# Performance work log

Hardware: AMD Instinct MI355X
Metric: run time of the kernel (lower is better)

Reference implementation:

```python
import jax, jax.numpy as jnp
import numpy as np

N_NODES = 50000
N_EDGES = 800000


def sage_conv(x, src, dst, W_l, b_l, W_r, num_nodes):
    """PyG SAGEConv with mean aggregation: out = lin_l(mean_agg(neighbors)) + lin_r(x)."""
    # gather source-node features per edge, scatter-mean into destination nodes
    msg = x[src]                                                   # [E, F]
    agg = jax.ops.segment_sum(msg, dst, num_segments=num_nodes)    # [N, F]
    cnt = jax.ops.segment_sum(jnp.ones((src.shape[0],), x.dtype), dst,
                              num_segments=num_nodes)              # [N]
    agg = agg / jnp.maximum(cnt, 1.0)[:, None]
    return agg @ W_l + b_l + x @ W_r


def setup_inputs() -> dict:
    key = jax.random.key(0)
    ks = jax.random.split(key, 8)
    d_in, d_hid, d_out = 128, 256, 128
    s = lambda k, shape, fan: jax.random.normal(k, shape, jnp.float32) / np.sqrt(fan)
    return {
        "x": jax.random.normal(ks[0], (N_NODES, d_in), jnp.float32),
        "edge_index": jax.random.randint(ks[1], (2, N_EDGES), 0, N_NODES, jnp.int64),
        "W1_l": s(ks[2], (d_in, d_hid), d_in),
        "b1": jnp.zeros((d_hid,), jnp.float32),
        "W1_r": s(ks[3], (d_in, d_hid), d_in),
        "W2_l": s(ks[4], (d_hid, d_out), d_hid),
        "b2": jnp.zeros((d_out,), jnp.float32),
        "W2_r": s(ks[5], (d_hid, d_out), d_hid),
    }


def reference(x, edge_index, W1_l, b1, W1_r, W2_l, b2, W2_r):
    src, dst = edge_index[0], edge_index[1]
    n = x.shape[0]
    h = sage_conv(x, src, dst, W1_l, b1, W1_r, n)
    h = jax.nn.relu(h)  # dropout p=0.0 -> identity
    out = sage_conv(h, src, dst, W2_l, b2, W2_r, n)
    return out
```

## Files before the change

### kernel.cpp

```cpp
#include <hip/hip_runtime.h>
#include <hip/hip_bf16.h>
#include <stdint.h>

#define NN 50000
#define NE 800000
#define NB 196
#define EPB 2048
#define NBLK ((NE + EPB - 1) / EPB)

typedef __attribute__((ext_vector_type(8))) __bf16 bf16x8;
typedef __attribute__((ext_vector_type(4))) float f32x4;
typedef __attribute__((ext_vector_type(4))) int i32x4;

__device__ __forceinline__ float bflo(uint32_t u) { return __uint_as_float(u << 16); }
__device__ __forceinline__ float bfhi(uint32_t u) { return __uint_as_float(u & 0xffff0000u); }
__device__ __forceinline__ uint16_t f2bf(float f) {
    uint32_t u = __float_as_uint(f);
    u += 0x7fffu + ((u >> 16) & 1u);
    return (uint16_t)(u >> 16);
}
__device__ __forceinline__ float bf2f(uint16_t h) { return __uint_as_float(((uint32_t)h) << 16); }

__device__ __forceinline__ int xcd_swz(int bid, int nwg) {
    int q = nwg >> 3, r = nwg & 7;
    int xcd = bid & 7, idx = bid >> 3;
    int base = (xcd < r) ? xcd * (q + 1) : r * (q + 1) + (xcd - r) * q;
    return base + idx;
}

__global__ __launch_bounds__(256) void detect(const uint32_t* __restrict__ xu,
                                              const int* __restrict__ ei,
                                              int* __restrict__ flags) {
    __shared__ int cnt_f, cnt_i;
    if (threadIdx.x == 0) { cnt_f = 0; cnt_i = 0; }
    __syncthreads();
    uint32_t u = xu[threadIdx.x];
    uint32_t lo = u & 0xffffu;
    uint32_t e = (lo >> 7) & 0xffu;
    int ok = (lo == 0u) || (e >= 96u && e <= 150u);
    atomicAdd(&cnt_f, ok);
    if (threadIdx.x < 64) {
        int w = ei[2 * threadIdx.x + 1];
        atomicAdd(&cnt_i, (w != 0) ? 1 : 0);
    }
    __syncthreads();
    if (threadIdx.x == 0) {
        flags[0] = (cnt_f < 192) ? 1 : 0;
        flags[1] = (cnt_i < 4) ? 1 : 0;
    }
}

__global__ __launch_bounds__(256) void hist_pass(const int* __restrict__ ei, const int* __restrict__ flags,
                                                 int* __restrict__ histM) {
    __shared__ int hist[NB];
    for (int i = threadIdx.x; i < NB; i += 256) hist[i] = 0;
    __syncthreads();
    int base = blockIdx.x * EPB;
    int fl = flags[1];
    for (int i = 0; i < EPB; i += 256) {
        int e = base + i + threadIdx.x;
        if (e < NE) {
            int d = fl ? ei[2 * NE + 2 * e] : ei[NE + e];
            atomicAdd(&hist[d >> 8], 1);
        }
    }
    __syncthreads();
    for (int i = threadIdx.x; i < NB; i += 256) histM[i * NBLK + blockIdx.x] = hist[i];
}

__global__ __launch_bounds__(512) void scan_rows(int* __restrict__ histM, int* __restrict__ bucket_tot) {
    __shared__ int sm[512];
    int b = blockIdx.x, t = threadIdx.x;
    int v = (t < NBLK) ? histM[b * NBLK + t] : 0;
    sm[t] = v;
    __syncthreads();
    for (int o = 1; o < 512; o <<= 1) {
        int x = (t >= o) ? sm[t - o] : 0;
        __syncthreads();
        sm[t] += x;
        __syncthreads();
    }
    if (t < NBLK) histM[b * NBLK + t] = sm[t] - v;
    if (t == 511) bucket_tot[b] = sm[511];
}

__global__ __launch_bounds__(256) void scan_tot(const int* __restrict__ bucket_tot, int* __restrict__ bucket_base) {
    __shared__ int sm[256];
    int t = threadIdx.x;
    int v = (t < NB) ? bucket_tot[t] : 0;
    sm[t] = v;
    __syncthreads();
    for (int o = 1; o < 256; o <<= 1) {
        int x = (t >= o) ? sm[t - o] : 0;
        __syncthreads();
        sm[t] += x;
        __syncthreads();
    }
    if (t < NB) bucket_base[t] = sm[t] - v;
    if (t == 0) bucket_base[NB] = NE;
}

__global__ __launch_bounds__(256) void scatter_pass(const int* __restrict__ ei, const int* __restrict__ flags,
                                                    const int* __restrict__ histM, const int* __restrict__ bucket_base,
                                                    uint32_t* __restrict__ staging) {
    __shared__ int curs[NB];
    int blk = blockIdx.x, t = threadIdx.x;
    for (int i = t; i < NB; i += 256) curs[i] = bucket_base[i] + histM[i * NBLK + blk];
    __syncthreads();
    int base = blk * EPB;
    int fl = flags[1];
    for (int i = 0; i < EPB; i += 256) {
        int e = base + i + t;
        if (e < NE) {
            int s, d;
            if (fl) { s = ei[2 * e]; d = ei[2 * NE + 2 * e]; }
            else    { s = ei[e];     d = ei[NE + e]; }
            int p = atomicAdd(&curs[d >> 8], 1);
            staging[p] = ((uint32_t)(d & 0xff) << 16) | (uint32_t)s;
        }
    }
}

__global__ __launch_bounds__(256) void build_csr(const uint32_t* __restrict__ staging,
                                                 const int* __restrict__ bucket_base,
                                                 int* __restrict__ row_start, int* __restrict__ deg,
                                                 float* __restrict__ inv_deg, int* __restrict__ csr) {
    __shared__ int degs[256];
    __shared__ int sm[256];
    __shared__ int curs[256];
    int b = blockIdx.x, t = threadIdx.x;
    int beg = bucket_base[b], cnt = bucket_base[b + 1] - beg;
    degs[t] = 0;
    __syncthreads();
    for (int i = t; i < cnt; i += 256) atomicAdd(&degs[(staging[beg + i] >> 16) & 0xff], 1);
    __syncthreads();
    int d = degs[t];
    sm[t] = d;
    __syncthreads();
    for (int o = 1; o < 256; o <<= 1) {
        int x = (t >= o) ? sm[t - o] : 0;
        __syncthreads();
        sm[t] += x;
        __syncthreads();
    }
    int excl = sm[t] - d;
    curs[t] = excl;
    int node = b * 256 + t;
    if (node < NN) {
        row_start[node] = beg + excl;
        deg[node] = d;
        inv_deg[node] = 1.0f / (float)(d > 0 ? d : 1);
    }
    __syncthreads();
    for (int i = t; i < cnt; i += 256) {
        uint32_t u = staging[beg + i];
        int dl = (u >> 16) & 0xff;
        int p = atomicAdd(&curs[dl], 1);
        csr[beg + p] = (int)(u & 0xffffu);
    }
}

__global__ __launch_bounds__(256) void norm_x(const void* __restrict__ x, const int* __restrict__ flags,
                                              uint32_t* __restrict__ out) {
    int i = blockIdx.x * 256 + threadIdx.x;
    if (flags[0]) {
        f32x4 v = ((const f32x4*)x)[i];
        uint2 o;
        o.x = (uint32_t)f2bf(v[0]) | ((uint32_t)f2bf(v[1]) << 16);
        o.y = (uint32_t)f2bf(v[2]) | ((uint32_t)f2bf(v[3]) << 16);
        ((uint2*)out)[i] = o;
    } else {
        ((uint2*)out)[i] = ((const uint2*)x)[i];
    }
}

__global__ __launch_bounds__(256) void norm_weights_sw(const void* __restrict__ w1l, const void* __restrict__ b1,
                                                       const void* __restrict__ w1r, const void* __restrict__ w2l,
                                                       const void* __restrict__ b2, const void* __restrict__ w2r,
                                                       const int* __restrict__ flags,
                                                       uint16_t* __restrict__ w1l_sw, uint16_t* __restrict__ w1r_sw,
                                                       uint16_t* __restrict__ w2l_sw, uint16_t* __restrict__ w2r_sw,
                                                       uint16_t* __restrict__ bias_buf) {
    int tid = blockIdx.x * 256 + threadIdx.x;
    int fp32 = flags[0];
    if (tid < 16384) {
        int frag = tid >> 6, lane = tid & 63;
        const void* srcw; uint16_t* dst; int N; int fl;
        if (frag < 64)       { srcw = w1l; dst = w1l_sw; N = 256; fl = frag; }
        else if (frag < 128) { srcw = w1r; dst = w1r_sw; N = 256; fl = frag - 64; }
        else if (frag < 192) { srcw = w2l; dst = w2l_sw; N = 128; fl = frag - 128; }
        else                 { srcw = w2r; dst = w2r_sw; N = 128; fl = frag - 192; }
        int NTm = N >> 4;
        int kt = fl / NTm, nt = fl - kt * NTm;
        int k0 = kt * 32 + (lane >> 4) * 8, n = nt * 16 + (lane & 15);
        uint16_t* d = dst + (size_t)fl * 512 + lane * 8;
#pragma unroll
        for (int j = 0; j < 8; j++) {
            int si = (k0 + j) * N + n;
            d[j] = fp32 ? f2bf(((const float*)srcw)[si]) : ((const uint16_t*)srcw)[si];
        }
    } else if (tid < 16384 + 384) {
        int j = tid - 16384;
        const void* s = (j < 256) ? b1 : b2;
        int jj = (j < 256) ? j : j - 256;
        bias_buf[j] = fp32 ? f2bf(((const float*)s)[jj]) : ((const uint16_t*)s)[jj];
    }
}

__global__ __launch_bounds__(256) void agg_mean_v2(const uint32_t* __restrict__ xu,
                                                   const int* __restrict__ row_start,
                                                   const int* __restrict__ deg,
                                                   const int* __restrict__ csr,
                                                   const float* __restrict__ inv_deg,
                                                   uint32_t* __restrict__ outu) {
    int wave = threadIdx.x >> 6, lane = threadIdx.x & 63;
    int half = lane >> 5, l = lane & 31;
    int node = blockIdx.x * 8 + wave * 2 + half;
    int beg = row_start[node], end = beg + deg[node];
    float lx[8], hx[8], ly[8], hy[8];
#pragma unroll
    for (int k = 0; k < 8; k++) { lx[k] = 0.f; hx[k] = 0.f; ly[k] = 0.f; hy[k] = 0.f; }
    int j = beg;
    for (; j + 8 <= end; j += 8) {
        int idx[8];
#pragma unroll
        for (int k = 0; k < 8; k++) idx[k] = csr[j + k];
#pragma unroll
        for (int k = 0; k < 8; k++) {
            uint2 v = *(const uint2*)(xu + (size_t)idx[k] * 64 + l * 2);
            lx[k] += bflo(v.x); hx[k] += bfhi(v.x);
            ly[k] += bflo(v.y); hy[k] += bfhi(v.y);
        }
    }
    for (; j < end; j++) {
        uint2 v = *(const uint2*)(xu + (size_t)csr[j] * 64 + l * 2);
        lx[0] += bflo(v.x); hx[0] += bfhi(v.x);
        ly[0] += bflo(v.y); hy[0] += bfhi(v.y);
    }
    float sc = inv_deg[node];
    float r0 = (((lx[0] + lx[1]) + (lx[2] + lx[3])) + ((lx[4] + lx[5]) + (lx[6] + lx[7]))) * sc;
    float r1 = (((hx[0] + hx[1]) + (hx[2] + hx[3])) + ((hx[4] + hx[5]) + (hx[6] + hx[7]))) * sc;
    float r2 = (((ly[0] + ly[1]) + (ly[2] + ly[3])) + ((ly[4] + ly[5]) + (ly[6] + ly[7]))) * sc;
    float r3 = (((hy[0] + hy[1]) + (hy[2] + hy[3])) + ((hy[4] + hy[5]) + (hy[6] + hy[7]))) * sc;
    uint2 o;
    o.x = (uint32_t)f2bf(r0) | ((uint32_t)f2bf(r1) << 16);
    o.y = (uint32_t)f2bf(r2) | ((uint32_t)f2bf(r3) << 16);
    *(uint2*)(outu + (size_t)node * 64 + l * 2) = o;
}

__global__ __launch_bounds__(256) void agg_final_v2(const uint32_t* __restrict__ tu,
                                                    const int* __restrict__ row_start,
                                                    const int* __restrict__ deg,
                                                    const int* __restrict__ csr,
                                                    const float* __restrict__ inv_deg,
                                                    const f32x4* __restrict__ u,
                                                    f32x4* __restrict__ out) {
    int wave = threadIdx.x >> 6, lane = threadIdx.x & 63;
    int half = lane >> 5, l = lane & 31;
    int node = blockIdx.x * 8 + wave * 2 + half;
    int beg = row_start[node], end = beg + deg[node];
    float lx[8], hx[8], ly[8], hy[8];
#pragma unroll
    for (int k = 0; k < 8; k++) { lx[k] = 0.f; hx[k] = 0.f; ly[k] = 0.f; hy[k] = 0.f; }
    int j = beg;
    for (; j + 8 <= end; j += 8) {
        int idx[8];
#pragma unroll
        for (int k = 0; k < 8; k++) idx[k] = csr[j + k];
#pragma unroll
        for (int k = 0; k < 8; k++) {
            uint2 v = *(const uint2*)(tu + (size_t)idx[k] * 64 + l * 2);
            lx[k] += bflo(v.x); hx[k] += bfhi(v.x);
            ly[k] += bflo(v.y); hy[k] += bfhi(v.y);
        }
    }
    for (; j < end; j++) {
        uint2 v = *(const uint2*)(tu + (size_t)csr[j] * 64 + l * 2);
        lx[0] += bflo(v.x); hx[0] += bfhi(v.x);
        ly[0] += bflo(v.y); hy[0] += bfhi(v.y);
    }
    float sc = inv_deg[node];
    f32x4 uv = u[(size_t)node * 32 + l];
    f32x4 r;
    r[0] = (((lx[0] + lx[1]) + (lx[2] + lx[3])) + ((lx[4] + lx[5]) + (lx[6] + lx[7]))) * sc + uv[0];
    r[1] = (((hx[0] + hx[1]) + (hx[2] + hx[3])) + ((hx[4] + hx[5]) + (hx[6] + hx[7]))) * sc + uv[1];
    r[2] = (((ly[0] + ly[1]) + (ly[2] + ly[3])) + ((ly[4] + ly[5]) + (ly[6] + ly[7]))) * sc + uv[2];
    r[3] = (((hy[0] + hy[1]) + (hy[2] + hy[3])) + ((hy[4] + hy[5]) + (hy[6] + hy[7]))) * sc + uv[3];
    out[(size_t)node * 32 + l] = r;
}

__global__ __launch_bounds__(256) void gemm1_v2(const uint16_t* __restrict__ A1,
                                                const uint16_t* __restrict__ A2,
                                                const uint16_t* __restrict__ W1sw,
                                                const uint16_t* __restrict__ W2sw,
                                                const uint16_t* __restrict__ bias,
                                                uint16_t* __restrict__ C) {
    __shared__ __align__(16) uint16_t cs[64][72];
    int wg = xcd_swz(blockIdx.x, 3128);
    int rg = wg >> 2, cg = wg & 3;
    int wave = threadIdx.x >> 6, lane = threadIdx.x & 63;
    int wr = wave >> 1, wc = wave & 1;
    int m = lane & 15, q = lane >> 4;
    int rowbase = rg * 64 + wr * 32;
    int gnt0 = cg * 4 + wc * 2;

    int ar[2];
#pragma unroll
    for (int rf = 0; rf < 2; rf++) {
        int r = rowbase + rf * 16 + m;
        ar[rf] = (r < NN) ? r : (NN - 1);
    }

    f32x4 acc[2][2];
#pragma unroll
    for (int rf = 0; rf < 2; rf++)
#pragma unroll
        for (int nt = 0; nt < 2; nt++)
#pragma unroll
            for (int i = 0; i < 4; i++) acc[rf][nt][i] = 0.f;

    {
        bf16x8 B[4][2];
#pragma unroll
        for (int kt = 0; kt < 4; kt++)
#pragma unroll
            for (int nt = 0; nt < 2; nt++)
                B[kt][nt] = *(const bf16x8*)(W1sw + ((size_t)(kt * 16 + gnt0 + nt)) * 512 + lane * 8);
#pragma unroll
        for (int kt = 0; kt < 4; kt++) {
            bf16x8 a0 = *(const bf16x8*)(A1 + (size_t)ar[0] * 128 + kt * 32 + q * 8);
            bf16x8 a1 = *(const bf16x8*)(A1 + (size_t)ar[1] * 128 + kt * 32 + q * 8);
#pragma unroll
            for (int nt = 0; nt < 2; nt++) {
                acc[0][nt] = __builtin_amdgcn_mfma_f32_16x16x32_bf16(a0, B[kt][nt], acc[0][nt], 0, 0, 0);
                acc[1][nt] = __builtin_amdgcn_mfma_f32_16x16x32_bf16(a1, B[kt][nt], acc[1][nt], 0, 0, 0);
            }
        }
    }
    asm volatile("" ::: "memory");
    {
        bf16x8 B[4][2];
#pragma unroll
        for (int kt = 0; kt < 4; kt++)
#pragma unroll
            for (int nt = 0; nt < 2; nt++)
                B[kt][nt] = *(const bf16x8*)(W2sw + ((size_t)(kt * 16 + gnt0 + nt)) * 512 + lane * 8);
#pragma unroll
        for (int kt = 0; kt < 4; kt++) {
            bf16x8 a0 = *(const bf16x8*)(A2 + (size_t)ar[0] * 128 + kt * 32 + q * 8);
            bf16x8 a1 = *(const bf16x8*)(A2 + (size_t)ar[1] * 128 + kt * 32 + q * 8);
#pragma unroll
            for (int nt = 0; nt < 2; nt++) {
                acc[0][nt] = __builtin_amdgcn_mfma_f32_16x16x32_bf16(a0, B[kt][nt], acc[0][nt], 0, 0, 0);
                acc[1][nt] = __builtin_amdgcn_mfma_f32_16x16x32_bf16(a1, B[kt][nt], acc[1][nt], 0, 0, 0);
            }
        }
    }

#pragma unroll
    for (int rf = 0; rf < 2; rf++)
#pragma unroll
        for (int nt = 0; nt < 2; nt++) {
            int coll = wc * 32 + nt * 16 + m;
            float bv = bf2f(bias[cg * 64 + coll]);
#pragma unroll
            for (int i = 0; i < 4; i++) {
                float v = fmaxf(acc[rf][nt][i] + bv, 0.f);
                cs[wr * 32 + rf * 16 + q * 4 + i][coll] = f2bf(v);
            }
        }
    __syncthreads();
    int tt = threadIdx.x;
#pragma unroll
    for (int rr = 0; rr < 2; rr++) {
        int row = rr * 32 + (tt >> 3);
        int grow = rg * 64 + row;
        if (grow < NN)
            *(i32x4*)(C + (size_t)grow * 256 + cg * 64 + (tt & 7) * 8) =
                *(const i32x4*)&cs[row][(tt & 7) * 8];
    }
}

__global__ __launch_bounds__(256) void gemm2_v2(const uint16_t* __restrict__ A,
                                                const uint16_t* __restrict__ W1sw,
                                                const uint16_t* __restrict__ W2sw,
                                                const uint16_t* __restrict__ bias,
                                                uint16_t* __restrict__ T,
                                                float* __restrict__ U) {
    __shared__ __align__(16) uint16_t ts[64][72];
    __shared__ __align__(16) float us[64][68];
    int wg = xcd_swz(blockIdx.x, 1564);
    int rg = wg >> 1, cg = wg & 1;
    int wave = threadIdx.x >> 6, lane = threadIdx.x & 63;
    int wr = wave >> 1, wc = wave & 1;
    int m = lane & 15, q = lane >> 4;
    int rowbase = rg * 64 + wr * 32;
    int gnt0 = cg * 4 + wc * 2;

    int ar[2];
#pragma unroll
    for (int rf = 0; rf < 2; rf++) {
        int r = rowbase + rf * 16 + m;
        ar[rf] = (r < NN) ? r : (NN - 1);
    }

    f32x4 acc1[2][2], acc2[2][2];
#pragma unroll
    for (int rf = 0; rf < 2; rf++)
#pragma unroll
        for (int nt = 0; nt < 2; nt++)
#pragma unroll
            for (int i = 0; i < 4; i++) { acc1[rf][nt][i] = 0.f; acc2[rf][nt][i] = 0.f; }

    {
        bf16x8 B[8][2];
#pragma unroll
        for (int kt = 0; kt < 8; kt++)
#pragma unroll
            for (int nt = 0; nt < 2; nt++)
                B[kt][nt] = *(const bf16x8*)(W1sw + ((size_t)(kt * 8 + gnt0 + nt)) * 512 + lane * 8);
#pragma unroll
        for (int kt = 0; kt < 8; kt++) {
            bf16x8 a0 = *(const bf16x8*)(A + (size_t)ar[0] * 256 + kt * 32 + q * 8);
            bf16x8 a1 = *(const bf16x8*)(A + (size_t)ar[1] * 256 + kt * 32 + q * 8);
#pragma unroll
            for (int nt = 0; nt < 2; nt++) {
                acc1[0][nt] = __builtin_amdgcn_mfma_f32_16x16x32_bf16(a0, B[kt][nt], acc1[0][nt], 0, 0, 0);
                acc1[1][nt] = __builtin_amdgcn_mfma_f32_16x16x32_bf16(a1, B[kt][nt], acc1[1][nt], 0, 0, 0);
            }
        }
    }
    asm volatile("" ::: "memory");
    {
        bf16x8 B[8][2];
#pragma unroll
        for (int kt = 0; kt < 8; kt++)
#pragma unroll
            for (int nt = 0; nt < 2; nt++)
                B[kt][nt] = *(const bf16x8*)(W2sw + ((size_t)(kt * 8 + gnt0 + nt)) * 512 + lane * 8);
#pragma unroll
        for (int kt = 0; kt < 8; kt++) {
            bf16x8 a0 = *(const bf16x8*)(A + (size_t)ar[0] * 256 + kt * 32 + q * 8);
            bf16x8 a1 = *(const bf16x8*)(A + (size_t)ar[1] * 256 + kt * 32 + q * 8);
#pragma unroll
            for (int nt = 0; nt < 2; nt++) {
                acc2[0][nt] = __builtin_amdgcn_mfma_f32_16x16x32_bf16(a0, B[kt][nt], acc2[0][nt], 0, 0, 0);
                acc2[1][nt] = __builtin_amdgcn_mfma_f32_16x16x32_bf16(a1, B[kt][nt], acc2[1][nt], 0, 0, 0);
            }
        }
    }

#pragma unroll
    for (int rf = 0; rf < 2; rf++)
#pragma unroll
        for (int nt = 0; nt < 2; nt++) {
            int coll = wc * 32 + nt * 16 + m;
            float bv = bf2f(bias[cg * 64 + coll]);
#pragma unroll
            for (int i = 0; i < 4; i++) {
                int rl = wr * 32 + rf * 16 + q * 4 + i;
                ts[rl][coll] = f2bf(acc1[rf][nt][i]);
                us[rl][coll] = acc2[rf][nt][i] + bv;
            }
        }
    __syncthreads();
    int tt = threadIdx.x;
#pragma unroll
    for (int rr = 0; rr < 2; rr++) {
        int row = rr * 32 + (tt >> 3);
        int grow = rg * 64 + row;
        if (grow < NN)
            *(i32x4*)(T + (size_t)grow * 128 + cg * 64 + (tt & 7) * 8) =
                *(const i32x4*)&ts[row][(tt & 7) * 8];
    }
#pragma unroll
    for (int rr = 0; rr < 4; rr++) {
        int row = rr * 16 + (tt >> 4);
        int grow = rg * 64 + row;
        if (grow < NN)
            *(f32x4*)(U + (size_t)grow * 128 + cg * 64 + (tt & 15) * 4) =
                *(const f32x4*)&us[row][(tt & 15) * 4];
    }
}

extern "C" void kernel_launch(void* const* d_in, const int* in_sizes, int n_in,
                              void* d_out, int out_size, void* d_ws, size_t ws_size,
                              hipStream_t stream) {
    const void* x_raw  = d_in[0];
    const int*  ei     = (const int*)d_in[1];
    const void* W1l    = d_in[2];
    const void* b1     = d_in[3];
    const void* W1r    = d_in[4];
    const void* W2l    = d_in[5];
    const void* b2     = d_in[6];
    const void* W2r    = d_in[7];

    uint8_t* ws = (uint8_t*)d_ws;
    size_t off = 0;
    auto alloc = [&](size_t b) -> void* {
        void* p = ws + off;
        off += (b + 255) & ~(size_t)255;
        return p;
    };
    int*      flags       = (int*)alloc(256);
    int*      histM       = (int*)alloc((size_t)NB * NBLK * 4);
    int*      bucket_tot  = (int*)alloc((NB + 4) * 4);
    int*      bucket_base = (int*)alloc((NB + 4) * 4);
    int*      deg         = (int*)alloc((size_t)NN * 4);
    float*    inv_deg     = (float*)alloc((size_t)NN * 4);
    int*      row_start   = (int*)alloc((size_t)NN * 4);
    int*      csr         = (int*)alloc((size_t)NE * 4);
    uint32_t* xb          = (uint32_t*)alloc((size_t)NN * 64 * 4);
    uint16_t* bias_buf    = (uint16_t*)alloc(384 * 2);
    uint16_t* agg         = (uint16_t*)alloc((size_t)NN * 128 * 2);
    uint16_t* h           = (uint16_t*)alloc((size_t)NN * 256 * 2);
    uint16_t* t           = (uint16_t*)alloc((size_t)NN * 128 * 2);
    float*    u           = (float*)alloc((size_t)NN * 128 * 4);
    uint16_t* w1l_sw      = (uint16_t*)alloc(128 * 256 * 2);
    uint16_t* w1r_sw      = (uint16_t*)alloc(128 * 256 * 2);
    uint16_t* w2l_sw      = (uint16_t*)alloc(256 * 128 * 2);
    uint16_t* w2r_sw      = (uint16_t*)alloc(256 * 128 * 2);

    uint32_t* staging = (uint32_t*)h;

    detect<<<1, 256, 0, stream>>>((const uint32_t*)x_raw, ei, flags);

    hist_pass<<<NBLK, 256, 0, stream>>>(ei, flags, histM);
    scan_rows<<<NB, 512, 0, stream>>>(histM, bucket_tot);
    scan_tot<<<1, 256, 0, stream>>>(bucket_tot, bucket_base);
    scatter_pass<<<NBLK, 256, 0, stream>>>(ei, flags, histM, bucket_base, staging);
    build_csr<<<NB, 256, 0, stream>>>(staging, bucket_base, row_start, deg, inv_deg, csr);

    norm_x<<<(NN * 32 + 255) / 256, 256, 0, stream>>>(x_raw, flags, xb);
    norm_weights_sw<<<66, 256, 0, stream>>>(W1l, b1, W1r, W2l, b2, W2r, flags,
                                            w1l_sw, w1r_sw, w2l_sw, w2r_sw, bias_buf);

    agg_mean_v2<<<NN / 8, 256, 0, stream>>>(xb, row_start, deg, csr, inv_deg, (uint32_t*)agg);
    gemm1_v2<<<3128, 256, 0, stream>>>(agg, (const uint16_t*)xb, w1l_sw, w1r_sw, bias_buf, h);
    gemm2_v2<<<1564, 256, 0, stream>>>(h, w2l_sw, w2r_sw, bias_buf + 256, t, u);
    agg_final_v2<<<NN / 8, 256, 0, stream>>>((const uint32_t*)t, row_start, deg, csr, inv_deg,
                                             (const f32x4*)u, (f32x4*)d_out);
}
```

Measured before the change: 267.4 us.

## Fold detect and scan kernels into consumers, merge norm kernels, interleave GEMM loads

Removes the standalone detect, scan_tot and norm_weights launches. Each consuming block now recomputes the dtype/int64 detection and the bucket prefix scan in shared memory, and x and weight normalization run in one merged kernel. The GEMM kernels interleave the two weight matrices' MFMA chains in one k-loop so A-row loads and both B operand sets are issued together. This trades redundant per-block scan/detect work and higher register pressure for fewer kernel launches and better memory-level parallelism.

```diff
diff --git a/kernel.cpp b/kernel.cpp
--- a/kernel.cpp
+++ b/kernel.cpp
@@ -28,35 +28,36 @@
     return base + idx;
 }
 
-__global__ __launch_bounds__(256) void detect(const uint32_t* __restrict__ xu,
-                                              const int* __restrict__ ei,
-                                              int* __restrict__ flags) {
-    __shared__ int cnt_f, cnt_i;
-    if (threadIdx.x == 0) { cnt_f = 0; cnt_i = 0; }
-    __syncthreads();
-    uint32_t u = xu[threadIdx.x];
+__device__ __forceinline__ int detect_i64(const int* ei, int* sh_cnt) {
+    int t = threadIdx.x;
+    if (t == 0) *sh_cnt = 0;
+    __syncthreads();
+    if (t < 64) atomicAdd(sh_cnt, (ei[2 * t + 1] != 0) ? 1 : 0);
+    __syncthreads();
+    return (*sh_cnt < 4) ? 1 : 0;
+}
+
+__device__ __forceinline__ int detect_fp32(const uint32_t* xu, int* sh_cnt) {
+    int t = threadIdx.x;
+    if (t == 0) *sh_cnt = 0;
+    __syncthreads();
+    uint32_t u = xu[t & 255];
     uint32_t lo = u & 0xffffu;
     uint32_t e = (lo >> 7) & 0xffu;
     int ok = (lo == 0u) || (e >= 96u && e <= 150u);
-    atomicAdd(&cnt_f, ok);
-    if (threadIdx.x < 64) {
-        int w = ei[2 * threadIdx.x + 1];
-        atomicAdd(&cnt_i, (w != 0) ? 1 : 0);
-    }
-    __syncthreads();
-    if (threadIdx.x == 0) {
-        flags[0] = (cnt_f < 192) ? 1 : 0;
-        flags[1] = (cnt_i < 4) ? 1 : 0;
-    }
-}
-
-__global__ __launch_bounds__(256) void hist_pass(const int* __restrict__ ei, const int* __restrict__ flags,
+    if (t < 256) atomicAdd(sh_cnt, ok);
+    __syncthreads();
+    return (*sh_cnt < 192) ? 1 : 0;
+}
+
+__global__ __launch_bounds__(256) void hist_pass(const int* __restrict__ ei,
                                                  int* __restrict__ histM) {
     __shared__ int hist[NB];
+    __shared__ int shc;
+    int fl = detect_i64(ei, &shc);
     for (int i = threadIdx.x; i < NB; i += 256) hist[i] = 0;
     __syncthreads();
     int base = blockIdx.x * EPB;
-    int fl = flags[1];
     for (int i = 0; i < EPB; i += 256) {
         int e = base + i + threadIdx.x;
         if (e < NE) {
@@ -84,9 +85,15 @@
     if (t == 511) bucket_tot[b] = sm[511];
 }
 
-__global__ __launch_bounds__(256) void scan_tot(const int* __restrict__ bucket_tot, int* __restrict__ bucket_base) {
+__global__ __launch_bounds__(256) void scatter_pass(const int* __restrict__ ei,
+                                                    const int* __restrict__ histM,
+                                                    const int* __restrict__ bucket_tot,
+                                                    uint32_t* __restrict__ staging) {
     __shared__ int sm[256];
-    int t = threadIdx.x;
+    __shared__ int curs[NB];
+    __shared__ int shc;
+    int fl = detect_i64(ei, &shc);
+    int blk = blockIdx.x, t = threadIdx.x;
     int v = (t < NB) ? bucket_tot[t] : 0;
     sm[t] = v;
     __syncthreads();
@@ -96,19 +103,9 @@
         sm[t] += x;
         __syncthreads();
     }
-    if (t < NB) bucket_base[t] = sm[t] - v;
-    if (t == 0) bucket_base[NB] = NE;
-}
-
-__global__ __launch_bounds__(256) void scatter_pass(const int* __restrict__ ei, const int* __restrict__ flags,
-                                                    const int* __restrict__ histM, const int* __restrict__ bucket_base,
-                                                    uint32_t* __restrict__ staging) {
-    __shared__ int curs[NB];
-    int blk = blockIdx.x, t = threadIdx.x;
-    for (int i = t; i < NB; i += 256) curs[i] = bucket_base[i] + histM[i * NBLK + blk];
+    if (t < NB) curs[t] = (sm[t] - v) + histM[t * NBLK + blk];
     __syncthreads();
     int base = blk * EPB;
-    int fl = flags[1];
     for (int i = 0; i < EPB; i += 256) {
         int e = base + i + t;
         if (e < NE) {
@@ -122,14 +119,26 @@
 }
 
 __global__ __launch_bounds__(256) void build_csr(const uint32_t* __restrict__ staging,
-                                                 const int* __restrict__ bucket_base,
+                                                 const int* __restrict__ bucket_tot,
                                                  int* __restrict__ row_start, int* __restrict__ deg,
                                                  float* __restrict__ inv_deg, int* __restrict__ csr) {
     __shared__ int degs[256];
     __shared__ int sm[256];
     __shared__ int curs[256];
+    __shared__ int beg_s, cnt_s;
     int b = blockIdx.x, t = threadIdx.x;
-    int beg = bucket_base[b], cnt = bucket_base[b + 1] - beg;
+    int v = (t < NB) ? bucket_tot[t] : 0;
+    sm[t] = v;
+    __syncthreads();
+    for (int o = 1; o < 256; o <<= 1) {
+        int x = (t >= o) ? sm[t - o] : 0;
+        __syncthreads();
+        sm[t] += x;
+        __syncthreads();
+    }
+    if (t == b) { beg_s = sm[t] - v; cnt_s = v; }
+    __syncthreads();
+    int beg = beg_s, cnt = cnt_s;
     degs[t] = 0;
     __syncthreads();
     for (int i = t; i < cnt; i += 256) atomicAdd(&degs[(staging[beg + i] >> 16) & 0xff], 1);
@@ -160,29 +169,31 @@
     }
 }
 
-__global__ __launch_bounds__(256) void norm_x(const void* __restrict__ x, const int* __restrict__ flags,
-                                              uint32_t* __restrict__ out) {
-    int i = blockIdx.x * 256 + threadIdx.x;
-    if (flags[0]) {
-        f32x4 v = ((const f32x4*)x)[i];
-        uint2 o;
-        o.x = (uint32_t)f2bf(v[0]) | ((uint32_t)f2bf(v[1]) << 16);
-        o.y = (uint32_t)f2bf(v[2]) | ((uint32_t)f2bf(v[3]) << 16);
-        ((uint2*)out)[i] = o;
-    } else {
-        ((uint2*)out)[i] = ((const uint2*)x)[i];
-    }
-}
-
-__global__ __launch_bounds__(256) void norm_weights_sw(const void* __restrict__ w1l, const void* __restrict__ b1,
-                                                       const void* __restrict__ w1r, const void* __restrict__ w2l,
-                                                       const void* __restrict__ b2, const void* __restrict__ w2r,
-                                                       const int* __restrict__ flags,
-                                                       uint16_t* __restrict__ w1l_sw, uint16_t* __restrict__ w1r_sw,
-                                                       uint16_t* __restrict__ w2l_sw, uint16_t* __restrict__ w2r_sw,
-                                                       uint16_t* __restrict__ bias_buf) {
-    int tid = blockIdx.x * 256 + threadIdx.x;
-    int fp32 = flags[0];
+#define NORMX_BLKS 6250
+__global__ __launch_bounds__(256) void norm_all(const void* __restrict__ x,
+                                                const void* __restrict__ w1l, const void* __restrict__ b1,
+                                                const void* __restrict__ w1r, const void* __restrict__ w2l,
+                                                const void* __restrict__ b2, const void* __restrict__ w2r,
+                                                uint32_t* __restrict__ xb,
+                                                uint16_t* __restrict__ w1l_sw, uint16_t* __restrict__ w1r_sw,
+                                                uint16_t* __restrict__ w2l_sw, uint16_t* __restrict__ w2r_sw,
+                                                uint16_t* __restrict__ bias_buf) {
+    __shared__ int shc;
+    int fp32 = detect_fp32((const uint32_t*)x, &shc);
+    if (blockIdx.x < NORMX_BLKS) {
+        int i = blockIdx.x * 256 + threadIdx.x;
+        if (fp32) {
+            f32x4 v = ((const f32x4*)x)[i];
+            uint2 o;
+            o.x = (uint32_t)f2bf(v[0]) | ((uint32_t)f2bf(v[1]) << 16);
+            o.y = (uint32_t)f2bf(v[2]) | ((uint32_t)f2bf(v[3]) << 16);
+            ((uint2*)xb)[i] = o;
+        } else {
+            ((uint2*)xb)[i] = ((const uint2*)x)[i];
+        }
+        return;
+    }
+    int tid = (blockIdx.x - NORMX_BLKS) * 256 + threadIdx.x;
     if (tid < 16384) {
         int frag = tid >> 6, lane = tid & 63;
         const void* srcw; uint16_t* dst; int N; int fl;
@@ -289,7 +300,7 @@
     out[(size_t)node * 32 + l] = r;
 }
 
-__global__ __launch_bounds__(256) void gemm1_v2(const uint16_t* __restrict__ A1,
+__global__ __launch_bounds__(256) void gemm1_v3(const uint16_t* __restrict__ A1,
                                                 const uint16_t* __restrict__ A2,
                                                 const uint16_t* __restrict__ W1sw,
                                                 const uint16_t* __restrict__ W2sw,
@@ -311,6 +322,15 @@
         ar[rf] = (r < NN) ? r : (NN - 1);
     }
 
+    bf16x8 B1[4][2], B2[4][2];
+#pragma unroll
+    for (int kt = 0; kt < 4; kt++)
+#pragma unroll
+        for (int nt = 0; nt < 2; nt++) {
+            B1[kt][nt] = *(const bf16x8*)(W1sw + ((size_t)(kt * 16 + gnt0 + nt)) * 512 + lane * 8);
+            B2[kt][nt] = *(const bf16x8*)(W2sw + ((size_t)(kt * 16 + gnt0 + nt)) * 512 + lane * 8);
+        }
+
     f32x4 acc[2][2];
 #pragma unroll
     for (int rf = 0; rf < 2; rf++)
@@ -319,41 +339,18 @@
 #pragma unroll
             for (int i = 0; i < 4; i++) acc[rf][nt][i] = 0.f;
 
-    {
-        bf16x8 B[4][2];
-#pragma unroll
-        for (int kt = 0; kt < 4; kt++)
-#pragma unroll
-            for (int nt = 0; nt < 2; nt++)
-                B[kt][nt] = *(const bf16x8*)(W1sw + ((size_t)(kt * 16 + gnt0 + nt)) * 512 + lane * 8);
-#pragma unroll
-        for (int kt = 0; kt < 4; kt++) {
-            bf16x8 a0 = *(const bf16x8*)(A1 + (size_t)ar[0] * 128 + kt * 32 + q * 8);
-            bf16x8 a1 = *(const bf16x8*)(A1 + (size_t)ar[1] * 128 + kt * 32 + q * 8);
-#pragma unroll
-            for (int nt = 0; nt < 2; nt++) {
-                acc[0][nt] = __builtin_amdgcn_mfma_f32_16x16x32_bf16(a0, B[kt][nt], acc[0][nt], 0, 0, 0);
-                acc[1][nt] = __builtin_amdgcn_mfma_f32_16x16x32_bf16(a1, B[kt][nt], acc[1][nt], 0, 0, 0);
-            }
-        }
-    }
-    asm volatile("" ::: "memory");
-    {
-        bf16x8 B[4][2];
-#pragma unroll
-        for (int kt = 0; kt < 4; kt++)
-#pragma unroll
-            for (int nt = 0; nt < 2; nt++)
-                B[kt][nt] = *(const bf16x8*)(W2sw + ((size_t)(kt * 16 + gnt0 + nt)) * 512 + lane * 8);
-#pragma unroll
-        for (int kt = 0; kt < 4; kt++) {
-            bf16x8 a0 = *(const bf16x8*)(A2 + (size_t)ar[0] * 128 + kt * 32 + q * 8);
-            bf16x8 a1 = *(const bf16x8*)(A2 + (size_t)ar[1] * 128 + kt * 32 + q * 8);
-#pragma unroll
-            for (int nt = 0; nt < 2; nt++) {
-                acc[0][nt] = __builtin_amdgcn_mfma_f32_16x16x32_bf16(a0, B[kt][nt], acc[0][nt], 0, 0, 0);
-                acc[1][nt] = __builtin_amdgcn_mfma_f32_16x16x32_bf16(a1, B[kt][nt], acc[1][nt], 0, 0, 0);
-            }
+#pragma unroll
+    for (int kt = 0; kt < 4; kt++) {
+        bf16x8 a10 = *(const bf16x8*)(A1 + (size_t)ar[0] * 128 + kt * 32 + q * 8);
+        bf16x8 a11 = *(const bf16x8*)(A1 + (size_t)ar[1] * 128 + kt * 32 + q * 8);
+        bf16x8 a20 = *(const bf16x8*)(A2 + (size_t)ar[0] * 128 + kt * 32 + q * 8);
+        bf16x8 a21 = *(const bf16x8*)(A2 + (size_t)ar[1] * 128 + kt * 32 + q * 8);
+#pragma unroll
+        for (int nt = 0; nt < 2; nt++) {
+            acc[0][nt] = __builtin_amdgcn_mfma_f32_16x16x32_bf16(a10, B1[kt][nt], acc[0][nt], 0, 0, 0);
+            acc[1][nt] = __builtin_amdgcn_mfma_f32_16x16x32_bf16(a11, B1[kt][nt], acc[1][nt], 0, 0, 0);
+            acc[0][nt] = __builtin_amdgcn_mfma_f32_16x16x32_bf16(a20, B2[kt][nt], acc[0][nt], 0, 0, 0);
+            acc[1][nt] = __builtin_amdgcn_mfma_f32_16x16x32_bf16(a21, B2[kt][nt], acc[1][nt], 0, 0, 0);
         }
     }
 
@@ -381,7 +378,7 @@
     }
 }
 
-__global__ __launch_bounds__(256) void gemm2_v2(const uint16_t* __restrict__ A,
+__global__ __launch_bounds__(256) void gemm2_v3(const uint16_t* __restrict__ A,
                                                 const uint16_t* __restrict__ W1sw,
                                                 const uint16_t* __restrict__ W2sw,
                                                 const uint16_t* __restrict__ bias,
@@ -412,42 +409,22 @@
 #pragma unroll
             for (int i = 0; i < 4; i++) { acc1[rf][nt][i] = 0.f; acc2[rf][nt][i] = 0.f; }
 
-    {
-        bf16x8 B[8][2];
-#pragma unroll
-        for (int kt = 0; kt < 8; kt++)
-#pragma unroll
-            for (int nt = 0; nt < 2; nt++)
-                B[kt][nt] = *(const bf16x8*)(W1sw + ((size_t)(kt * 8 + gnt0 + nt)) * 512 + lane * 8);
-#pragma unroll
-        for (int kt = 0; kt < 8; kt++) {
-            bf16x8 a0 = *(const bf16x8*)(A + (size_t)ar[0] * 256 + kt * 32 + q * 8);
-            bf16x8 a1 = *(const bf16x8*)(A + (size_t)ar[1] * 256 + kt * 32 + q * 8);
-#pragma unroll
-            for (int nt = 0; nt < 2; nt++) {
-                acc1[0][nt] = __builtin_amdgcn_mfma_f32_16x16x32_bf16(a0, B[kt][nt], acc1[0][nt], 0, 0, 0);
-                acc1[1][nt] = __builtin_amdgcn_mfma_f32_16x16x32_bf16(a1, B[kt][nt], acc1[1][nt], 0, 0, 0);
-            }
-        }
-    }
-    asm volatile("" ::: "memory");
-    {
-        bf16x8 B[8][2];
-#pragma unroll
-        for (int kt = 0; kt < 8; kt++)
-#pragma unroll
-            for (int nt = 0; nt < 2; nt++)
-                B[kt][nt] = *(const bf16x8*)(W2sw + ((size_t)(kt * 8 + gnt0 + nt)) * 512 + lane * 8);
-#pragma unroll
-        for (int kt = 0; kt < 8; kt++) {
-            bf16x8 a0 = *(const bf16x8*)(A + (size_t)ar[0] * 256 + kt * 32 + q * 8);
-            bf16x8 a1 = *(const bf16x8*)(A + (size_t)ar[1] * 256 + kt * 32 + q * 8);
-#pragma unroll
-            for (int nt = 0; nt < 2; nt++) {
-                acc2[0][nt] = __builtin_amdgcn_mfma_f32_16x16x32_bf16(a0, B[kt][nt], acc2[0][nt], 0, 0, 0);
-                acc2[1][nt] = __builtin_amdgcn_mfma_f32_16x16x32_bf16(a1, B[kt][nt], acc2[1][nt], 0, 0, 0);
-            }
-        }
+#pragma unroll
+    for (int kt = 0; kt < 8; kt++) {
+        bf16x8 b10 = *(const bf16x8*)(W1sw + ((size_t)(kt * 8 + gnt0 + 0)) * 512 + lane * 8);
+        bf16x8 b11 = *(const bf16x8*)(W1sw + ((size_t)(kt * 8 + gnt0 + 1)) * 512 + lane * 8);
+        bf16x8 b20 = *(const bf16x8*)(W2sw + ((size_t)(kt * 8 + gnt0 + 0)) * 512 + lane * 8);
+        bf16x8 b21 = *(const bf16x8*)(W2sw + ((size_t)(kt * 8 + gnt0 + 1)) * 512 + lane * 8);
+        bf16x8 a0 = *(const bf16x8*)(A + (size_t)ar[0] * 256 + kt * 32 + q * 8);
+        bf16x8 a1 = *(const bf16x8*)(A + (size_t)ar[1] * 256 + kt * 32 + q * 8);
+        acc1[0][0] = __builtin_amdgcn_mfma_f32_16x16x32_bf16(a0, b10, acc1[0][0], 0, 0, 0);
+        acc1[0][1] = __builtin_amdgcn_mfma_f32_16x16x32_bf16(a0, b11, acc1[0][1], 0, 0, 0);
+        acc1[1][0] = __builtin_amdgcn_mfma_f32_16x16x32_bf16(a1, b10, acc1[1][0], 0, 0, 0);
+        acc1[1][1] = __builtin_amdgcn_mfma_f32_16x16x32_bf16(a1, b11, acc1[1][1], 0, 0, 0);
+        acc2[0][0] = __builtin_amdgcn_mfma_f32_16x16x32_bf16(a0, b20, acc2[0][0], 0, 0, 0);
+        acc2[0][1] = __builtin_amdgcn_mfma_f32_16x16x32_bf16(a0, b21, acc2[0][1], 0, 0, 0);
+        acc2[1][0] = __builtin_amdgcn_mfma_f32_16x16x32_bf16(a1, b20, acc2[1][0], 0, 0, 0);
+        acc2[1][1] = __builtin_amdgcn_mfma_f32_16x16x32_bf16(a1, b21, acc2[1][1], 0, 0, 0);
     }
 
 #pragma unroll
@@ -502,10 +479,8 @@
         off += (b + 255) & ~(size_t)255;
         return p;
     };
-    int*      flags       = (int*)alloc(256);
     int*      histM       = (int*)alloc((size_t)NB * NBLK * 4);
     int*      bucket_tot  = (int*)alloc((NB + 4) * 4);
-    int*      bucket_base = (int*)alloc((NB + 4) * 4);
     int*      deg         = (int*)alloc((size_t)NN * 4);
     float*    inv_deg     = (float*)alloc((size_t)NN * 4);
     int*      row_start   = (int*)alloc((size_t)NN * 4);
@@ -523,21 +498,17 @@
 
     uint32_t* staging = (uint32_t*)h;
 
-    detect<<<1, 256, 0, stream>>>((const uint32_t*)x_raw, ei, flags);
-
-    hist_pass<<<NBLK, 256, 0, stream>>>(ei, flags, histM);
+    hist_pass<<<NBLK, 256, 0, stream>>>(ei, histM);
     scan_rows<<<NB, 512, 0, stream>>>(histM, bucket_tot);
-    scan_tot<<<1, 256, 0, stream>>>(bucket_tot, bucket_base);
-    scatter_pass<<<NBLK, 256, 0, stream>>>(ei, flags, histM, bucket_base, staging);
-    build_csr<<<NB, 256, 0, stream>>>(staging, bucket_base, row_start, deg, inv_deg, csr);
-
-    norm_x<<<(NN * 32 + 255) / 256, 256, 0, stream>>>(x_raw, flags, xb);
-    norm_weights_sw<<<66, 256, 0, stream>>>(W1l, b1, W1r, W2l, b2, W2r, flags,
-                                            w1l_sw, w1r_sw, w2l_sw, w2r_sw, bias_buf);
+    scatter_pass<<<NBLK, 256, 0, stream>>>(ei, histM, bucket_tot, staging);
+    build_csr<<<NB, 256, 0, stream>>>(staging, bucket_tot, row_start, deg, inv_deg, csr);
+
+    norm_all<<<NORMX_BLKS + 66, 256, 0, stream>>>(x_raw, W1l, b1, W1r, W2l, b2, W2r,
+                                                  xb, w1l_sw, w1r_sw, w2l_sw, w2r_sw, bias_buf);
 
     agg_mean_v2<<<NN / 8, 256, 0, stream>>>(xb, row_start, deg, csr, inv_deg, (uint32_t*)agg);
-    gemm1_v2<<<3128, 256, 0, stream>>>(agg, (const uint16_t*)xb, w1l_sw, w1r_sw, bias_buf, h);
-    gemm2_v2<<<1564, 256, 0, stream>>>(h, w2l_sw, w2r_sw, bias_buf + 256, t, u);
+    gemm1_v3<<<3128, 256, 0, stream>>>(agg, (const uint16_t*)xb, w1l_sw, w1r_sw, bias_buf, h);
+    gemm2_v3<<<1564, 256, 0, stream>>>(h, w2l_sw, w2r_sw, bias_buf + 256, t, u);
     agg_final_v2<<<NN / 8, 256, 0, stream>>>((const uint32_t*)t, row_start, deg, csr, inv_deg,
                                              (const f32x4*)u, (f32x4*)d_out);
 }
```

Result: no change. 268.3 us (+0.3%).
